# Performance work log

Measured on AMD Instinct MI355X. Metric: run time of the kernel, lower is better.

The kernel has to match this reference:

```python
import jax, jax.numpy as jnp
import numpy as np

MARGIN = 2.0


def setup_inputs() -> dict:
    key = jax.random.key(0)
    k1, k2 = jax.random.split(key)
    predict = jax.random.normal(k1, (8192, 2048, 1, 1), dtype=jnp.float32)
    gt = jax.random.randint(k2, (8192, 1), 0, 751, dtype=jnp.int64)
    return {"predict": predict, "gt": gt}


def reference(predict, gt):
    # predict: [B, 2048, 1, 1] -> [B, D]
    p = predict.reshape(predict.shape[0], -1)
    b, d = p.shape
    # pairwise squared L2 distance / dim, via GEMM (||a||^2 + ||b||^2 - 2 a.b)
    sq = jnp.sum(p * p, axis=1)  # [B]
    d2 = (sq[:, None] + sq[None, :] - 2.0 * (p @ p.T))
    d2 = jnp.maximum(d2, 0.0) / d  # clamp tiny negatives from GEMM roundoff
    g = gt.reshape(-1)
    label = (g[:, None] == g[None, :]).astype(p.dtype)  # [B, B]
    term = label * d2 + (1.0 - label) * jax.nn.relu(MARGIN - d2)
    # original loop sums over j >= i (diagonal contributes 0: same label, dist 0)
    mask = jnp.triu(jnp.ones((b, b), dtype=bool))
    loss = jnp.sum(jnp.where(mask, term, 0.0))
    return 2.0 * loss / (b * (b - 1))
```

## Files before the change

kernel.cpp:

```cpp
#include <hip/hip_runtime.h>
#include <stdint.h>

#define NROWS 8192
#define DIM   2048
#define MARGIN 2.0f
#define SCALEQ (127.0f / 6.0f)
#define S2     ((6.0f / 127.0f) * (6.0f / 127.0f))

#define BT      128
#define BKB     128
#define NKT     (DIM / BKB)
#define NTR     (NROWS / BT)
#define NTILES  (NTR * (NTR + 1) / 2)
#define BOFF    16384

typedef __attribute__((ext_vector_type(4)))  int  int4v;
typedef __attribute__((ext_vector_type(16))) int  int16v;
typedef unsigned char uchar;

__device__ __forceinline__ void decode_tile(int bid, int* ti, int* tj) {
    float fn = (float)NTR + 0.5f;
    int r = (int)(fn - sqrtf(fn * fn - 2.0f * (float)bid));
    if (r < 0) r = 0;
    if (r >= NTR) r = NTR - 1;
    while ((r + 1) * NTR - ((r + 1) * r) / 2 <= bid) ++r;
    while (r * NTR - (r * (r - 1)) / 2 > bid) --r;
    *ti = r;
    *tj = r + (bid - (r * NTR - (r * (r - 1)) / 2));
}

__device__ __forceinline__ uint pack4(float4 v) {
    int q0 = (int)__builtin_rintf(v.x * SCALEQ);
    int q1 = (int)__builtin_rintf(v.y * SCALEQ);
    int q2 = (int)__builtin_rintf(v.z * SCALEQ);
    int q3 = (int)__builtin_rintf(v.w * SCALEQ);
    q0 = min(max(q0, -127), 127); q1 = min(max(q1, -127), 127);
    q2 = min(max(q2, -127), 127); q3 = min(max(q3, -127), 127);
    return (uint)(q0 & 0xFF) | ((uint)(q1 & 0xFF) << 8) |
           ((uint)(q2 & 0xFF) << 16) | ((uint)(q3 & 0xFF) << 24);
}

__global__ __launch_bounds__(256) void prep_kernel(const float* __restrict__ p,
                                                   uchar* __restrict__ pb,
                                                   float* __restrict__ sq) {
    int row = blockIdx.x;
    int t = threadIdx.x;
    const float4* prow = (const float4*)(p + (size_t)row * DIM);
    uint* qrow = (uint*)(pb + (size_t)row * DIM);
    float4 a = prow[t];
    float4 b = prow[t + 256];
    float s = a.x * a.x + a.y * a.y + a.z * a.z + a.w * a.w
            + b.x * b.x + b.y * b.y + b.z * b.z + b.w * b.w;
    qrow[t] = pack4(a);
    qrow[t + 256] = pack4(b);
#pragma unroll
    for (int o = 32; o > 0; o >>= 1) s += __shfl_down(s, o, 64);
    __shared__ float wsums[4];
    int lane = t & 63, wvv = t >> 6;
    if (lane == 0) wsums[wvv] = s;
    __syncthreads();
    if (t == 0) sq[row] = wsums[0] + wsums[1] + wsums[2] + wsums[3];
}

__device__ __forceinline__ void stage_m(const uchar* __restrict__ pb,
                                        uchar* lds, int t, int isB,
                                        int rbase, int tid) {
    if (t >= NKT) t = NKT - 1;
    const uchar* g0 = pb + (size_t)rbase * DIM + t * BKB;
    uchar* l0 = lds + (isB ? BOFF : 0);
#pragma unroll
    for (int r = 0; r < 4; ++r) {
        int row = r * 32 + (tid >> 3);
        int c8 = (tid & 7) ^ ((tid >> 3) & 7);
        const uchar* g = g0 + (size_t)row * DIM + c8 * 16;
        uchar* l = l0 + r * 4096 + (tid >> 6) * 1024;
        __builtin_amdgcn_global_load_lds(
            (const __attribute__((address_space(1))) uint32_t*)g,
            (__attribute__((address_space(3))) uint32_t*)l, 16, 0, 0);
    }
}

#define BARF()   do { __builtin_amdgcn_s_barrier(); \
                      asm volatile("" ::: "memory"); } while (0)
#define WAITL()  asm volatile("s_waitcnt lgkmcnt(0)" ::: "memory")
#define WAITV0() asm volatile("s_waitcnt vmcnt(0)" ::: "memory")
#define PRIO1()  __builtin_amdgcn_s_setprio(1)
#define PRIO0()  __builtin_amdgcn_s_setprio(0)
#define SB0()    __builtin_amdgcn_sched_barrier(0)

#define READ_A(MT)                                                             \
    _Pragma("unroll") for (int s = 0; s < 4; ++s) {                            \
        int rl = wr * 64 + (MT) * 32 + (lane & 31);                            \
        af[MT][s] = *(const int4v*)&lds[rl * 128 +                             \
                     (((2 * s + kh) ^ (lane & 7)) * 16)];                      \
    }

#define READ_B(NT)                                                             \
    _Pragma("unroll") for (int s = 0; s < 4; ++s) {                            \
        int rl = wc * 64 + (NT) * 32 + (lane & 31);                            \
        bf[NT][s] = *(const int4v*)&lds[BOFF + rl * 128 +                      \
                     (((2 * s + kh) ^ (lane & 7)) * 16)];                      \
    }

#define MFMA_ROW(MT)                                                           \
    _Pragma("unroll") for (int s = 0; s < 4; ++s)                              \
    _Pragma("unroll") for (int nt = 0; nt < 2; ++nt)                           \
        acc[MT][nt] = __builtin_amdgcn_mfma_i32_32x32x32_i8(                   \
            af[MT][s], bf[nt][s], acc[MT][nt], 0, 0, 0);

#define STEP(T)                                                                \
    {                                                                          \
        READ_A(0);                                                             \
        READ_B(0);                                                             \
        READ_B(1);                                                             \
        PRIO1(); MFMA_ROW(0); PRIO0();                                         \
        READ_A(1);                                                             \
        WAITL(); BARF();                                                       \
        stage_m(pb, lds, (T) + 1, 0, ibase, tid);                              \
        stage_m(pb, lds, (T) + 1, 1, jbase, tid);                              \
        SB0();                                                                 \
        PRIO1(); MFMA_ROW(1); PRIO0();                                         \
        WAITV0(); BARF();                                                      \
    }

__global__ __launch_bounds__(256) void tile2_kernel(
    const uchar* __restrict__ pb, const float* __restrict__ sq,
    const int* __restrict__ gt, double* __restrict__ accum) {

    __shared__ uchar lds[32768];
    __shared__ float wsum[4];

    int f = (int)blockIdx.x;
    int bid = (f & 7) * (NTILES / 8) + (f >> 3);

    int ti, tj;
    decode_tile(bid, &ti, &tj);

    const int tid = threadIdx.x;
    const int lane = tid & 63;
    const int kh = lane >> 5;
    const int wv = tid >> 6;
    const int wr = wv >> 1;
    const int wc = wv & 1;
    const int ibase = ti * BT;
    const int jbase = tj * BT;

    int16v acc[2][2] = {};
    int4v af[2][4];
    int4v bf[2][4];

    stage_m(pb, lds, 0, 0, ibase, tid);
    stage_m(pb, lds, 0, 1, jbase, tid);
    WAITV0();
    BARF();

#pragma unroll 1
    for (int s0 = 0; s0 < NKT; ++s0) {
        STEP(s0);
    }

    const float invd = 1.0f / (float)DIM;
    float lsum = 0.f;
    {
        int j0 = jbase + wc * 64 + (lane & 31);
        float sqj[2]; int gj[2];
#pragma unroll
        for (int nt = 0; nt < 2; ++nt) { int j = j0 + nt * 32; sqj[nt] = sq[j]; gj[nt] = gt[j]; }
        const float wb = (ti != tj) ? 2.0f : 1.0f;
#pragma unroll
        for (int mt = 0; mt < 2; ++mt) {
#pragma unroll
            for (int q = 0; q < 4; ++q) {
#pragma unroll
                for (int rr = 0; rr < 4; ++rr) {
                    int i = ibase + wr * 64 + mt * 32 + rr + 8 * q + 4 * kh;
                    float sqi = sq[i];
                    int gi = gt[i];
#pragma unroll
                    for (int nt = 0; nt < 2; ++nt) {
                        int j = j0 + nt * 32;
                        float dot = S2 * (float)acc[mt][nt][q * 4 + rr];
                        float d2 = fmaxf(sqi + sqj[nt] - 2.0f * dot, 0.0f) * invd;
                        float term = (gi == gj[nt]) ? d2 : fmaxf(MARGIN - d2, 0.0f);
                        float w = wb;
                        if (ti == tj && i == j) w = 2.0f;
                        lsum += w * term;
                    }
                }
            }
        }
    }

#pragma unroll
    for (int o = 32; o > 0; o >>= 1) lsum += __shfl_down(lsum, o, 64);
    if (lane == 0) wsum[wv] = lsum;
    __syncthreads();
    if (tid == 0)
        atomicAdd(accum, (double)(wsum[0] + wsum[1] + wsum[2] + wsum[3]));
}

__global__ void finalize_kernel(const double* __restrict__ accum,
                                float* __restrict__ out) {
    if (threadIdx.x == 0)
        out[0] = (float)(accum[0] * (1.0 / ((double)NROWS * (double)(NROWS - 1))));
}

extern "C" void kernel_launch(void* const* d_in, const int* in_sizes, int n_in,
                              void* d_out, int out_size, void* d_ws, size_t ws_size,
                              hipStream_t stream) {
    (void)in_sizes; (void)n_in; (void)out_size; (void)ws_size;
    const float* p = (const float*)d_in[0];
    const int* gt = (const int*)d_in[1];
    float* out = (float*)d_out;

    uchar* pb = (uchar*)d_ws;
    size_t off = (size_t)NROWS * DIM;
    float* sq = (float*)((char*)d_ws + off);
    off += (size_t)NROWS * sizeof(float);
    double* accum = (double*)((char*)d_ws + off);

    (void)hipMemsetAsync(accum, 0, sizeof(double), stream);
    prep_kernel<<<NROWS, 256, 0, stream>>>(p, pb, sq);
    tile2_kernel<<<NTILES, 256, 0, stream>>>(pb, sq, gt, accum);
    finalize_kernel<<<1, 64, 0, stream>>>(accum, out);
}
```

Before: 114.2 us.

## Switch to 128x256 tiles over upper triangle plus separate diagonal tiles

Replaces the 128x128 triangular tile decomposition with 1024 rectangular 128x256 tiles (each wave covers 128x64), plus 32 special 128x128 diagonal tiles for the odd diagonal blocks. The larger tiles raise MFMA work per byte loaded from LDS and global memory, and the tile count drops from 2080 to 1056. The grid swizzle and the tile decode change to match. Launch bounds now request 2 blocks per CU and LDS grows to 48KB, so register pressure from the 4x2 accumulators could limit occupancy.

```diff
diff --git a/kernel.cpp b/kernel.cpp
--- a/kernel.cpp
+++ b/kernel.cpp
@@ -7,27 +7,15 @@
 #define SCALEQ (127.0f / 6.0f)
 #define S2     ((6.0f / 127.0f) * (6.0f / 127.0f))
 
-#define BT      128
 #define BKB     128
 #define NKT     (DIM / BKB)
-#define NTR     (NROWS / BT)
-#define NTILES  (NTR * (NTR + 1) / 2)
+#define NDIAG   32
+#define NFULL   1024
 #define BOFF    16384
 
 typedef __attribute__((ext_vector_type(4)))  int  int4v;
 typedef __attribute__((ext_vector_type(16))) int  int16v;
 typedef unsigned char uchar;
-
-__device__ __forceinline__ void decode_tile(int bid, int* ti, int* tj) {
-    float fn = (float)NTR + 0.5f;
-    int r = (int)(fn - sqrtf(fn * fn - 2.0f * (float)bid));
-    if (r < 0) r = 0;
-    if (r >= NTR) r = NTR - 1;
-    while ((r + 1) * NTR - ((r + 1) * r) / 2 <= bid) ++r;
-    while (r * NTR - (r * (r - 1)) / 2 > bid) --r;
-    *ti = r;
-    *tj = r + (bid - (r * NTR - (r * (r - 1)) / 2));
-}
 
 __device__ __forceinline__ uint pack4(float4 v) {
     int q0 = (int)__builtin_rintf(v.x * SCALEQ);
@@ -62,14 +50,14 @@
     if (t == 0) sq[row] = wsums[0] + wsums[1] + wsums[2] + wsums[3];
 }
 
-__device__ __forceinline__ void stage_m(const uchar* __restrict__ pb,
-                                        uchar* lds, int t, int isB,
-                                        int rbase, int tid) {
+template<int NCH, int ROFF>
+__device__ __forceinline__ void stage_r(const uchar* __restrict__ pb,
+                                        uchar* lds, int t, int rbase, int tid) {
     if (t >= NKT) t = NKT - 1;
     const uchar* g0 = pb + (size_t)rbase * DIM + t * BKB;
-    uchar* l0 = lds + (isB ? BOFF : 0);
-#pragma unroll
-    for (int r = 0; r < 4; ++r) {
+    uchar* l0 = lds + ROFF;
+#pragma unroll
+    for (int r = 0; r < NCH; ++r) {
         int row = r * 32 + (tid >> 3);
         int c8 = (tid & 7) ^ ((tid >> 3) & 7);
         const uchar* g = g0 + (size_t)row * DIM + c8 * 16;
@@ -88,92 +76,103 @@
 #define PRIO0()  __builtin_amdgcn_s_setprio(0)
 #define SB0()    __builtin_amdgcn_sched_barrier(0)
 
-#define READ_A(MT)                                                             \
-    _Pragma("unroll") for (int s = 0; s < 4; ++s) {                            \
-        int rl = wr * 64 + (MT) * 32 + (lane & 31);                            \
-        af[MT][s] = *(const int4v*)&lds[rl * 128 +                             \
-                     (((2 * s + kh) ^ (lane & 7)) * 16)];                      \
-    }
-
-#define READ_B(NT)                                                             \
-    _Pragma("unroll") for (int s = 0; s < 4; ++s) {                            \
-        int rl = wc * 64 + (NT) * 32 + (lane & 31);                            \
-        bf[NT][s] = *(const int4v*)&lds[BOFF + rl * 128 +                      \
-                     (((2 * s + kh) ^ (lane & 7)) * 16)];                      \
-    }
-
-#define MFMA_ROW(MT)                                                           \
+#define RD_AF(MT)                                                              \
+    _Pragma("unroll") for (int s = 0; s < 4; ++s)                              \
+        af[MT][s] = *(const int4v*)&lds[                                       \
+            (((MT) * 32 + (lane & 31)) * 128) +                                \
+            (((2 * s + kh) ^ (lane & 7)) * 16)];
+
+#define RD_BF(NT)                                                              \
+    _Pragma("unroll") for (int s = 0; s < 4; ++s)                              \
+        bf[NT][s] = *(const int4v*)&lds[BOFF +                                 \
+            ((wv * 64 + (NT) * 32 + (lane & 31)) * 128) +                      \
+            (((2 * s + kh) ^ (lane & 7)) * 16)];
+
+#define MFMA_MT(MT)                                                            \
     _Pragma("unroll") for (int s = 0; s < 4; ++s)                              \
     _Pragma("unroll") for (int nt = 0; nt < 2; ++nt)                           \
         acc[MT][nt] = __builtin_amdgcn_mfma_i32_32x32x32_i8(                   \
             af[MT][s], bf[nt][s], acc[MT][nt], 0, 0, 0);
 
-#define STEP(T)                                                                \
-    {                                                                          \
-        READ_A(0);                                                             \
-        READ_B(0);                                                             \
-        READ_B(1);                                                             \
-        PRIO1(); MFMA_ROW(0); PRIO0();                                         \
-        READ_A(1);                                                             \
-        WAITL(); BARF();                                                       \
-        stage_m(pb, lds, (T) + 1, 0, ibase, tid);                              \
-        stage_m(pb, lds, (T) + 1, 1, jbase, tid);                              \
-        SB0();                                                                 \
-        PRIO1(); MFMA_ROW(1); PRIO0();                                         \
-        WAITV0(); BARF();                                                      \
-    }
-
-__global__ __launch_bounds__(256) void tile2_kernel(
+#define RD_DA(MT)                                                              \
+    _Pragma("unroll") for (int s = 0; s < 4; ++s)                              \
+        af[MT][s] = *(const int4v*)&lds[                                       \
+            ((wr * 64 + (MT) * 32 + (lane & 31)) * 128) +                      \
+            (((2 * s + kh) ^ (lane & 7)) * 16)];
+
+#define RD_DB(NT)                                                              \
+    _Pragma("unroll") for (int s = 0; s < 4; ++s)                              \
+        bf[NT][s] = *(const int4v*)&lds[BOFF +                                 \
+            ((wc * 64 + (NT) * 32 + (lane & 31)) * 128) +                      \
+            (((2 * s + kh) ^ (lane & 7)) * 16)];
+
+#define MFMA_D(MT)                                                             \
+    _Pragma("unroll") for (int s = 0; s < 4; ++s)                              \
+    _Pragma("unroll") for (int nt = 0; nt < 2; ++nt)                           \
+        acc[MT][nt] = __builtin_amdgcn_mfma_i32_32x32x32_i8(                   \
+            af[MT][s], bf[nt][s], acc[MT][nt], 0, 0, 0);
+
+__global__ __launch_bounds__(256, 2) void tile2_kernel(
     const uchar* __restrict__ pb, const float* __restrict__ sq,
     const int* __restrict__ gt, double* __restrict__ accum) {
 
-    __shared__ uchar lds[32768];
+    __shared__ uchar lds[49152];
     __shared__ float wsum[4];
 
-    int f = (int)blockIdx.x;
-    int bid = (f & 7) * (NTILES / 8) + (f >> 3);
-
-    int ti, tj;
-    decode_tile(bid, &ti, &tj);
-
+    const int bx = (int)blockIdx.x;
     const int tid = threadIdx.x;
     const int lane = tid & 63;
     const int kh = lane >> 5;
     const int wv = tid >> 6;
-    const int wr = wv >> 1;
-    const int wc = wv & 1;
-    const int ibase = ti * BT;
-    const int jbase = tj * BT;
-
-    int16v acc[2][2] = {};
-    int4v af[2][4];
-    int4v bf[2][4];
-
-    stage_m(pb, lds, 0, 0, ibase, tid);
-    stage_m(pb, lds, 0, 1, jbase, tid);
-    WAITV0();
-    BARF();
-
-#pragma unroll 1
-    for (int s0 = 0; s0 < NKT; ++s0) {
-        STEP(s0);
-    }
 
     const float invd = 1.0f / (float)DIM;
     float lsum = 0.f;
-    {
-        int j0 = jbase + wc * 64 + (lane & 31);
+
+    if (bx >= NDIAG) {
+        int f = bx - NDIAG;
+        f = (f & 7) * 128 + (f >> 3);
+        int J = (int)sqrtf((float)f + 0.5f);
+        while ((J + 1) * (J + 1) <= f) ++J;
+        while (J * J > f) --J;
+        const int ti = f - J * J;
+        const int ibase = ti * 128;
+        const int jbase = J * 256;
+
+        int16v acc[4][2] = {};
+        int4v af[4][4];
+        int4v bf[2][4];
+
+        stage_r<4, 0>(pb, lds, 0, ibase, tid);
+        stage_r<8, BOFF>(pb, lds, 0, jbase, tid);
+        WAITV0();
+        BARF();
+
+#pragma unroll 1
+        for (int t = 0; t < NKT; ++t) {
+            RD_AF(0); RD_AF(1);
+            RD_BF(0); RD_BF(1);
+            RD_AF(2); RD_AF(3);
+            PRIO1(); MFMA_MT(0); MFMA_MT(1); PRIO0();
+            WAITL(); BARF();
+            stage_r<4, 0>(pb, lds, t + 1, ibase, tid);
+            stage_r<8, BOFF>(pb, lds, t + 1, jbase, tid);
+            SB0();
+            PRIO1(); MFMA_MT(2); MFMA_MT(3); PRIO0();
+            WAITV0();
+            BARF();
+        }
+
+        int j0 = jbase + wv * 64 + (lane & 31);
         float sqj[2]; int gj[2];
 #pragma unroll
         for (int nt = 0; nt < 2; ++nt) { int j = j0 + nt * 32; sqj[nt] = sq[j]; gj[nt] = gt[j]; }
-        const float wb = (ti != tj) ? 2.0f : 1.0f;
-#pragma unroll
-        for (int mt = 0; mt < 2; ++mt) {
+#pragma unroll
+        for (int mt = 0; mt < 4; ++mt) {
 #pragma unroll
             for (int q = 0; q < 4; ++q) {
 #pragma unroll
                 for (int rr = 0; rr < 4; ++rr) {
-                    int i = ibase + wr * 64 + mt * 32 + rr + 8 * q + 4 * kh;
+                    int i = ibase + mt * 32 + rr + 8 * q + 4 * kh;
                     float sqi = sq[i];
                     int gi = gt[i];
 #pragma unroll
@@ -182,8 +181,59 @@
                         float dot = S2 * (float)acc[mt][nt][q * 4 + rr];
                         float d2 = fmaxf(sqi + sqj[nt] - 2.0f * dot, 0.0f) * invd;
                         float term = (gi == gj[nt]) ? d2 : fmaxf(MARGIN - d2, 0.0f);
-                        float w = wb;
-                        if (ti == tj && i == j) w = 2.0f;
+                        float w = ((j >> 7) != ti) ? 2.0f : ((i == j) ? 2.0f : 1.0f);
+                        lsum += w * term;
+                    }
+                }
+            }
+        }
+    } else {
+        const int td = 2 * bx + 1;
+        const int ibase = td * 128;
+        const int wr = wv >> 1;
+        const int wc = wv & 1;
+
+        int16v acc[2][2] = {};
+        int4v af[2][4], bf[2][4];
+
+        stage_r<4, 0>(pb, lds, 0, ibase, tid);
+        stage_r<4, BOFF>(pb, lds, 0, ibase, tid);
+        WAITV0();
+        BARF();
+
+#pragma unroll 1
+        for (int t = 0; t < NKT; ++t) {
+            RD_DA(0); RD_DB(0); RD_DB(1); RD_DA(1);
+            PRIO1(); MFMA_D(0); PRIO0();
+            WAITL(); BARF();
+            stage_r<4, 0>(pb, lds, t + 1, ibase, tid);
+            stage_r<4, BOFF>(pb, lds, t + 1, ibase, tid);
+            SB0();
+            PRIO1(); MFMA_D(1); PRIO0();
+            WAITV0();
+            BARF();
+        }
+
+        int j0 = ibase + wc * 64 + (lane & 31);
+        float sqj[2]; int gj[2];
+#pragma unroll
+        for (int nt = 0; nt < 2; ++nt) { int j = j0 + nt * 32; sqj[nt] = sq[j]; gj[nt] = gt[j]; }
+#pragma unroll
+        for (int mt = 0; mt < 2; ++mt) {
+#pragma unroll
+            for (int q = 0; q < 4; ++q) {
+#pragma unroll
+                for (int rr = 0; rr < 4; ++rr) {
+                    int i = ibase + wr * 64 + mt * 32 + rr + 8 * q + 4 * kh;
+                    float sqi = sq[i];
+                    int gi = gt[i];
+#pragma unroll
+                    for (int nt = 0; nt < 2; ++nt) {
+                        int j = j0 + nt * 32;
+                        float dot = S2 * (float)acc[mt][nt][q * 4 + rr];
+                        float d2 = fmaxf(sqi + sqj[nt] - 2.0f * dot, 0.0f) * invd;
+                        float term = (gi == gj[nt]) ? d2 : fmaxf(MARGIN - d2, 0.0f);
+                        float w = (i == j) ? 2.0f : 1.0f;
                         lsum += w * term;
                     }
                 }
@@ -221,6 +271,6 @@
 
     (void)hipMemsetAsync(accum, 0, sizeof(double), stream);
     prep_kernel<<<NROWS, 256, 0, stream>>>(p, pb, sq);
-    tile2_kernel<<<NTILES, 256, 0, stream>>>(pb, sq, gt, accum);
+    tile2_kernel<<<NDIAG + NFULL, 256, 0, stream>>>(pb, sq, gt, accum);
     finalize_kernel<<<1, 64, 0, stream>>>(accum, out);
 }
```

New measurement: 115.2 us. No clear change (+0.9%).

## Double-buffer LDS to prefetch two K-tiles ahead in int8 GEMM loop

Applied to the files above, without the earlier changes.

Moves the K-loop from a single LDS buffer to two buffers, issuing global-to-LDS loads two tiles ahead and waiting only until the older batch has landed (vmcnt(8)) rather than draining all loads. The aim is to hide global memory latency behind the MFMA work. In exchange, LDS use doubles to 64KB per block, which may cut occupancy. Out-of-range prefetches at the tail reload earlier tiles into the same-parity buffer, which costs redundant traffic.

```diff
diff --git a/kernel.cpp b/kernel.cpp
--- a/kernel.cpp
+++ b/kernel.cpp
@@ -12,6 +12,7 @@
 #define NKT     (DIM / BKB)
 #define NTR     (NROWS / BT)
 #define NTILES  (NTR * (NTR + 1) / 2)
+#define BUFSZ   32768
 #define BOFF    16384
 
 typedef __attribute__((ext_vector_type(4)))  int  int4v;
@@ -65,9 +66,9 @@
 __device__ __forceinline__ void stage_m(const uchar* __restrict__ pb,
                                         uchar* lds, int t, int isB,
                                         int rbase, int tid) {
-    if (t >= NKT) t = NKT - 1;
+    if (t >= NKT) t -= 2;
     const uchar* g0 = pb + (size_t)rbase * DIM + t * BKB;
-    uchar* l0 = lds + (isB ? BOFF : 0);
+    uchar* l0 = lds + (t & 1) * BUFSZ + (isB ? BOFF : 0);
 #pragma unroll
     for (int r = 0; r < 4; ++r) {
         int row = r * 32 + (tid >> 3);
@@ -83,22 +84,23 @@
 #define BARF()   do { __builtin_amdgcn_s_barrier(); \
                       asm volatile("" ::: "memory"); } while (0)
 #define WAITL()  asm volatile("s_waitcnt lgkmcnt(0)" ::: "memory")
+#define WAITV8() asm volatile("s_waitcnt vmcnt(8)" ::: "memory")
 #define WAITV0() asm volatile("s_waitcnt vmcnt(0)" ::: "memory")
 #define PRIO1()  __builtin_amdgcn_s_setprio(1)
 #define PRIO0()  __builtin_amdgcn_s_setprio(0)
 #define SB0()    __builtin_amdgcn_sched_barrier(0)
 
-#define READ_A(MT)                                                             \
+#define READ_A(MT, BUFO)                                                       \
     _Pragma("unroll") for (int s = 0; s < 4; ++s) {                            \
         int rl = wr * 64 + (MT) * 32 + (lane & 31);                            \
-        af[MT][s] = *(const int4v*)&lds[rl * 128 +                             \
+        af[MT][s] = *(const int4v*)&lds[(BUFO) + rl * 128 +                    \
                      (((2 * s + kh) ^ (lane & 7)) * 16)];                      \
     }
 
-#define READ_B(NT)                                                             \
+#define READ_B(NT, BUFO)                                                       \
     _Pragma("unroll") for (int s = 0; s < 4; ++s) {                            \
         int rl = wc * 64 + (NT) * 32 + (lane & 31);                            \
-        bf[NT][s] = *(const int4v*)&lds[BOFF + rl * 128 +                      \
+        bf[NT][s] = *(const int4v*)&lds[(BUFO) + BOFF + rl * 128 +             \
                      (((2 * s + kh) ^ (lane & 7)) * 16)];                      \
     }
 
@@ -108,26 +110,26 @@
         acc[MT][nt] = __builtin_amdgcn_mfma_i32_32x32x32_i8(                   \
             af[MT][s], bf[nt][s], acc[MT][nt], 0, 0, 0);
 
-#define STEP(T)                                                                \
+#define STEP(T, BUFO)                                                          \
     {                                                                          \
-        READ_A(0);                                                             \
-        READ_B(0);                                                             \
-        READ_B(1);                                                             \
+        READ_A(0, BUFO);                                                       \
+        READ_B(0, BUFO);                                                       \
+        READ_B(1, BUFO);                                                       \
         PRIO1(); MFMA_ROW(0); PRIO0();                                         \
-        READ_A(1);                                                             \
+        READ_A(1, BUFO);                                                       \
         WAITL(); BARF();                                                       \
-        stage_m(pb, lds, (T) + 1, 0, ibase, tid);                              \
-        stage_m(pb, lds, (T) + 1, 1, jbase, tid);                              \
+        stage_m(pb, lds, (T) + 2, 0, ibase, tid);                              \
+        stage_m(pb, lds, (T) + 2, 1, jbase, tid);                              \
         SB0();                                                                 \
         PRIO1(); MFMA_ROW(1); PRIO0();                                         \
-        WAITV0(); BARF();                                                      \
+        WAITV8(); BARF();                                                      \
     }
 
 __global__ __launch_bounds__(256) void tile2_kernel(
     const uchar* __restrict__ pb, const float* __restrict__ sq,
     const int* __restrict__ gt, double* __restrict__ accum) {
 
-    __shared__ uchar lds[32768];
+    __shared__ uchar lds[2 * BUFSZ];
     __shared__ float wsum[4];
 
     int f = (int)blockIdx.x;
@@ -151,13 +153,17 @@
 
     stage_m(pb, lds, 0, 0, ibase, tid);
     stage_m(pb, lds, 0, 1, jbase, tid);
+    stage_m(pb, lds, 1, 0, ibase, tid);
+    stage_m(pb, lds, 1, 1, jbase, tid);
+    WAITV8();
+    BARF();
+
+#pragma unroll 1
+    for (int s0 = 0; s0 < NKT; s0 += 2) {
+        STEP(s0, 0);
+        STEP(s0 + 1, BUFSZ);
+    }
     WAITV0();
-    BARF();
-
-#pragma unroll 1
-    for (int s0 = 0; s0 < NKT; ++s0) {
-        STEP(s0);
-    }
 
     const float invd = 1.0f / (float)DIM;
     float lsum = 0.f;
```

Result: slower. 121.7 us (+6.6%).

## Split K-step fragment reads into halves to cut registers and raise occupancy

Applied to the files above, without the earlier changes.

Each K step now reads the A/B fragments from LDS in two half-K chunks instead of one full-K chunk, and issues the MFMAs for each half. This shrinks the live fragment registers, and the launch bounds now request 4 blocks per SM. The aim is higher occupancy and better latency hiding. In exchange, the MFMA chains between LDS reads are shorter and more LDS-read waits are exposed inside a step.

```diff
diff --git a/kernel.cpp b/kernel.cpp
--- a/kernel.cpp
+++ b/kernel.cpp
@@ -88,42 +88,59 @@
 #define PRIO0()  __builtin_amdgcn_s_setprio(0)
 #define SB0()    __builtin_amdgcn_sched_barrier(0)
 
-#define READ_A(MT)                                                             \
-    _Pragma("unroll") for (int s = 0; s < 4; ++s) {                            \
-        int rl = wr * 64 + (MT) * 32 + (lane & 31);                            \
-        af[MT][s] = *(const int4v*)&lds[rl * 128 +                             \
-                     (((2 * s + kh) ^ (lane & 7)) * 16)];                      \
-    }
-
-#define READ_B(NT)                                                             \
-    _Pragma("unroll") for (int s = 0; s < 4; ++s) {                            \
-        int rl = wc * 64 + (NT) * 32 + (lane & 31);                            \
-        bf[NT][s] = *(const int4v*)&lds[BOFF + rl * 128 +                      \
-                     (((2 * s + kh) ^ (lane & 7)) * 16)];                      \
-    }
-
-#define MFMA_ROW(MT)                                                           \
-    _Pragma("unroll") for (int s = 0; s < 4; ++s)                              \
+#define RD_A2(DST, SB)                                                         \
+    _Pragma("unroll") for (int mt = 0; mt < 2; ++mt)                           \
+    _Pragma("unroll") for (int sp = 0; sp < 2; ++sp) {                         \
+        int rl = wr * 64 + mt * 32 + (lane & 31);                              \
+        DST[mt][sp] = *(const int4v*)&lds[rl * 128 +                           \
+            (((2 * ((SB) + sp) + kh) ^ (lane & 7)) * 16)];                     \
+    }
+
+#define RD_B2(DST, SB)                                                         \
     _Pragma("unroll") for (int nt = 0; nt < 2; ++nt)                           \
-        acc[MT][nt] = __builtin_amdgcn_mfma_i32_32x32x32_i8(                   \
-            af[MT][s], bf[nt][s], acc[MT][nt], 0, 0, 0);
+    _Pragma("unroll") for (int sp = 0; sp < 2; ++sp) {                         \
+        int rl = wc * 64 + nt * 32 + (lane & 31);                              \
+        DST[nt][sp] = *(const int4v*)&lds[BOFF + rl * 128 +                    \
+            (((2 * ((SB) + sp) + kh) ^ (lane & 7)) * 16)];                     \
+    }
 
 #define STEP(T)                                                                \
     {                                                                          \
-        READ_A(0);                                                             \
-        READ_B(0);                                                             \
-        READ_B(1);                                                             \
-        PRIO1(); MFMA_ROW(0); PRIO0();                                         \
-        READ_A(1);                                                             \
-        WAITL(); BARF();                                                       \
-        stage_m(pb, lds, (T) + 1, 0, ibase, tid);                              \
-        stage_m(pb, lds, (T) + 1, 1, jbase, tid);                              \
-        SB0();                                                                 \
-        PRIO1(); MFMA_ROW(1); PRIO0();                                         \
-        WAITV0(); BARF();                                                      \
-    }
-
-__global__ __launch_bounds__(256) void tile2_kernel(
+        {                                                    \
+            int4v a0[2][2], b0[2][2];                                          \
+            RD_A2(a0, 0); RD_B2(b0, 0);                                        \
+            PRIO1();                                                           \
+            _Pragma("unroll") for (int sp = 0; sp < 2; ++sp)                   \
+            _Pragma("unroll") for (int mt = 0; mt < 2; ++mt)                   \
+            _Pragma("unroll") for (int nt = 0; nt < 2; ++nt)                   \
+                acc[mt][nt] = __builtin_amdgcn_mfma_i32_32x32x32_i8(           \
+                    a0[mt][sp], b0[nt][sp], acc[mt][nt], 0, 0, 0);             \
+            PRIO0();                                                           \
+        }                                                                      \
+        {                                                    \
+            int4v a1[2][2], b1[2][2];                                          \
+            RD_A2(a1, 2); RD_B2(b1, 2);                                        \
+            PRIO1();                                                           \
+            _Pragma("unroll") for (int sp = 0; sp < 2; ++sp)                   \
+            _Pragma("unroll") for (int nt = 0; nt < 2; ++nt)                   \
+                acc[0][nt] = __builtin_amdgcn_mfma_i32_32x32x32_i8(            \
+                    a1[0][sp], b1[nt][sp], acc[0][nt], 0, 0, 0);               \
+            PRIO0();                                                           \
+            WAITL(); BARF();                                                   \
+            stage_m(pb, lds, (T) + 1, 0, ibase, tid);                          \
+            stage_m(pb, lds, (T) + 1, 1, jbase, tid);                          \
+            SB0();                                                             \
+            PRIO1();                                                           \
+            _Pragma("unroll") for (int sp = 0; sp < 2; ++sp)                   \
+            _Pragma("unroll") for (int nt = 0; nt < 2; ++nt)                   \
+                acc[1][nt] = __builtin_amdgcn_mfma_i32_32x32x32_i8(            \
+                    a1[1][sp], b1[nt][sp], acc[1][nt], 0, 0, 0);               \
+            PRIO0();                                                           \
+            WAITV0(); BARF();                                                  \
+        }                                                                      \
+    }
+
+__global__ __launch_bounds__(256, 4) void tile2_kernel(
     const uchar* __restrict__ pb, const float* __restrict__ sq,
     const int* __restrict__ gt, double* __restrict__ accum) {
 
@@ -146,8 +163,6 @@
     const int jbase = tj * BT;
 
     int16v acc[2][2] = {};
-    int4v af[2][4];
-    int4v bf[2][4];
 
     stage_m(pb, lds, 0, 0, ibase, tid);
     stage_m(pb, lds, 0, 1, jbase, tid);
```

After: 114.8 us. Within noise of the previous version (+0.5%).
